# Performance work log

Measured on AMD Instinct MI355X. Metric: run time of the kernel, lower is better.

Reference implementation:

```python
import jax, jax.numpy as jnp
import numpy as np

N = 100000        # nodes
E = 3200000       # random edges (avg degree 32); self-loops added in reference
IN, HID, HEADS, OUT = 10, 32, 2, 4
NEG_SLOPE = 0.2   # PyG GATConv default leaky_relu slope


def setup_inputs() -> dict:
    key = jax.random.key(0)
    ks = jax.random.split(key, 16)
    s = 0.1
    return {
        "x": jax.random.normal(ks[0], (N, IN), jnp.float32),
        "edge_index": jax.random.randint(ks[1], (2, E), 0, N),
        "W1": jax.random.normal(ks[2], (IN, HEADS * HID), jnp.float32) * s,
        "a1s": jax.random.normal(ks[3], (HEADS, HID), jnp.float32) * s,
        "a1d": jax.random.normal(ks[4], (HEADS, HID), jnp.float32) * s,
        "b1": jnp.zeros((HEADS * HID,), jnp.float32),
        "W2": jax.random.normal(ks[5], (HEADS * HID, HEADS * HID), jnp.float32) * s,
        "a2s": jax.random.normal(ks[6], (HEADS, HID), jnp.float32) * s,
        "a2d": jax.random.normal(ks[7], (HEADS, HID), jnp.float32) * s,
        "b2": jnp.zeros((HEADS * HID,), jnp.float32),
        "W3": jax.random.normal(ks[8], (HEADS * HID, OUT), jnp.float32) * s,
        "a3s": jax.random.normal(ks[9], (1, OUT), jnp.float32) * s,
        "a3d": jax.random.normal(ks[10], (1, OUT), jnp.float32) * s,
        "b3": jnp.zeros((OUT,), jnp.float32),
    }


def gat_layer(x, src, dst, W, a_src, a_dst, b, concat):
    """One PyG-style GATConv (shared src/dst linear, self-loops already in src/dst)."""
    heads, oc = a_src.shape
    h = (x @ W).reshape(-1, heads, oc)                    # [N, H, C]
    asc = jnp.einsum('nhc,hc->nh', h, a_src)              # [N, H]
    adc = jnp.einsum('nhc,hc->nh', h, a_dst)              # [N, H]
    e = jax.nn.leaky_relu(asc[src] + adc[dst], NEG_SLOPE) # [Etot, H]
    m = jax.ops.segment_max(e, dst, num_segments=N)       # segment softmax over dst
    ex = jnp.exp(e - m[dst])
    z = jax.ops.segment_sum(ex, dst, num_segments=N)
    alpha = ex / z[dst]                                   # [Etot, H]
    out = jax.ops.segment_sum(h[src] * alpha[:, :, None], dst, num_segments=N)
    out = out.reshape(-1, heads * oc) if concat else out.mean(axis=1)
    return out + b


def reference(x, edge_index, W1, a1s, a1d, b1, W2, a2s, a2d, b2, W3, a3s, a3d, b3):
    loops = jnp.arange(N)
    src = jnp.concatenate([edge_index[0], loops])
    dst = jnp.concatenate([edge_index[1], loops])
    h = jax.nn.relu(gat_layer(x, src, dst, W1, a1s, a1d, b1, True))
    h = jax.nn.relu(gat_layer(h, src, dst, W2, a2s, a2d, b2, True))
    h = gat_layer(h, src, dst, W3, a3s, a3d, b3, False)
    return jax.nn.sigmoid(h) * 100.0
```

## Files before the change

kernel.cpp:

```cpp
#include <hip/hip_runtime.h>
#include <hip/hip_bf16.h>
#include <math.h>

#define NEG_SLOPE 0.2f
#define PSHIFT 8
#define PSIZE 256
#define NPARTS_MAX 392
#define B1 768
#define CELL_CAP 32
#define PCAP 10240
#define LCSR_CAP 10240

typedef int vint2 __attribute__((ext_vector_type(2)));
typedef int vint4 __attribute__((ext_vector_type(4)));
typedef short bf16x8 __attribute__((ext_vector_type(8)));
typedef float floatx4 __attribute__((ext_vector_type(4)));

__device__ __forceinline__ float lrelu(float v) { return fmaxf(v, NEG_SLOPE * v); }

__device__ __forceinline__ unsigned short f2bf(float f) {
    unsigned int b = __float_as_uint(f);
    b += 0x7fffu + ((b >> 16) & 1u);
    return (unsigned short)(b >> 16);
}
__device__ __forceinline__ float bf2f(unsigned short u) {
    return __uint_as_float((unsigned int)u << 16);
}

__global__ void k_part(const int* __restrict__ src, const int* __restrict__ dst, int E,
                       int* __restrict__ pairs, int* __restrict__ ptot, int nparts) {
    __shared__ int stage[NPARTS_MAX * CELL_CAP];
    __shared__ int lcnt[NPARTS_MAX];
    int tid = threadIdx.x, blk = blockIdx.x;
    for (int i = tid; i < nparts; i += 256) lcnt[i] = 0;
    __syncthreads();
    int per = ((E + B1 * 4 - 1) / (B1 * 4)) * 4;
    int s = blk * per, e = min(E, s + per);
    bool al = ((E & 3) == 0);
    for (int i0 = s + tid * 4; i0 < e; i0 += 1024) {
        int dv[4], sv[4], nv;
        if (al && i0 + 4 <= e) {
            vint4 d4 = __builtin_nontemporal_load((const vint4*)(dst + i0));
            vint4 s4 = __builtin_nontemporal_load((const vint4*)(src + i0));
            dv[0] = d4.x; dv[1] = d4.y; dv[2] = d4.z; dv[3] = d4.w;
            sv[0] = s4.x; sv[1] = s4.y; sv[2] = s4.z; sv[3] = s4.w;
            nv = 4;
        } else {
            nv = min(4, e - i0);
            for (int k = 0; k < nv; ++k) {
                dv[k] = __builtin_nontemporal_load(dst + i0 + k);
                sv[k] = __builtin_nontemporal_load(src + i0 + k);
            }
        }
        for (int k = 0; k < nv; ++k) {
            int p = dv[k] >> PSHIFT;
            int pos = atomicAdd(&lcnt[p], 1);
            if (pos < CELL_CAP)
                stage[p * CELL_CAP + pos] = (sv[k] << PSHIFT) | (dv[k] & (PSIZE - 1));
        }
    }
    __syncthreads();
    for (int p = tid; p < nparts; p += 256) {
        int tgt = min(lcnt[p], CELL_CAP);
        if (tgt == 0) continue;
        int base = atomicAdd(&ptot[p], tgt);
        if (base + tgt > PCAP) tgt = max(0, PCAP - base);
        int* gp = pairs + (size_t)p * PCAP + base;
        const int* sp = &stage[p * CELL_CAP];
        for (int j = 0; j < tgt; ++j) gp[j] = sp[j];
    }
}

__global__ void k_pscan(const int* __restrict__ ptot, int* __restrict__ pbase,
                        int* __restrict__ row, int nparts, int N) {
    __shared__ int sh[512];
    int tid = threadIdx.x;
    int v = (tid < nparts) ? min(ptot[tid], PCAP) : 0;
    sh[tid] = v;
    __syncthreads();
    for (int off = 1; off < 512; off <<= 1) {
        int t = (tid >= off) ? sh[tid - off] : 0;
        __syncthreads();
        sh[tid] += t;
        __syncthreads();
    }
    if (tid < nparts) pbase[tid] = sh[tid] - v;
    if (tid == nparts - 1) row[N] = sh[tid];
}

__global__ void k_scat2(const int* __restrict__ pairs, const int* __restrict__ ptot,
                        const int* __restrict__ pbase, int* __restrict__ row,
                        int* __restrict__ csr, int N) {
    __shared__ int lcsr[LCSR_CAP];
    __shared__ int lhist[PSIZE], lcur[PSIZE];
    int part = blockIdx.x;
    int lo = part << PSHIFT;
    int npart = min(PSIZE, N - lo);
    int tid = threadIdx.x;
    int cnt = min(ptot[part], PCAP);
    const int* seg = pairs + (size_t)part * PCAP;
    for (int i = tid; i < PSIZE; i += 1024) lhist[i] = 0;
    __syncthreads();
    for (int i = tid; i < cnt; i += 1024)
        atomicAdd(&lhist[__builtin_nontemporal_load(&seg[i]) & (PSIZE - 1)], 1);
    __syncthreads();
    if (tid < PSIZE) lcur[tid] = lhist[tid];
    __syncthreads();
    for (int off = 1; off < PSIZE; off <<= 1) {
        int t = 0;
        if (tid < PSIZE && tid >= off) t = lcur[tid - off];
        __syncthreads();
        if (tid < PSIZE) lcur[tid] += t;
        __syncthreads();
    }
    int pb = pbase[part];
    if (tid < npart) row[lo + tid] = pb + lcur[tid] - lhist[tid];
    if (tid < PSIZE) lcur[tid] -= lhist[tid];
    __syncthreads();
    for (int i = tid; i < cnt; i += 1024) {
        int v = __builtin_nontemporal_load(&seg[i]);
        int pos = atomicAdd(&lcur[v & (PSIZE - 1)], 1);
        if (pos < LCSR_CAP) lcsr[pos] = (unsigned)v >> PSHIFT;
    }
    __syncthreads();
    for (int i = tid; i < cnt; i += 1024)
        csr[pb + i] = lcsr[i];
}

__global__ void k_lin1(const float* __restrict__ x, const float* __restrict__ W,
                       const float* __restrict__ as_, const float* __restrict__ ad_,
                       unsigned short* __restrict__ hb, float* __restrict__ asc,
                       float* __restrict__ adc, int N) {
    __shared__ float sW[10 * 64];
    int tid = threadIdx.x;
    for (int i = tid; i < 640; i += 256) sW[i] = W[i];
    __syncthreads();
    int wid = tid >> 6, lane = tid & 63;
    int n = blockIdx.x * 4 + wid;
    if (n >= N) return;
    float acc = 0.f;
#pragma unroll
    for (int k = 0; k < 10; ++k) acc += x[n * 10 + k] * sW[k * 64 + lane];
    hb[(size_t)n * 64 + lane] = f2bf(acc);
    int head = lane >> 5, cc = lane & 31;
    float rs = acc * as_[lane];
    float rd = acc * ad_[lane];
#pragma unroll
    for (int m = 16; m >= 1; m >>= 1) {
        rs += __shfl_xor(rs, m, 64);
        rd += __shfl_xor(rd, m, 64);
    }
    if (cc == 0) { asc[n * 2 + head] = rs; adc[n * 2 + head] = rd; }
}

__global__ void k_lin2(const float* __restrict__ yin, const float* __restrict__ W,
                       const float* __restrict__ as_, const float* __restrict__ ad_,
                       unsigned short* __restrict__ hb, float* __restrict__ asc,
                       float* __restrict__ adc, int N) {
    __shared__ unsigned short sW[64 * 64];
    int tid = threadIdx.x;
    for (int i = tid; i < 4096; i += 256) sW[i] = f2bf(W[i]);
    __syncthreads();
    int wid = tid >> 6, lane = tid & 63;
    int quad = lane >> 4, col = lane & 15;
    bf16x8 bfr[4][2];
#pragma unroll
    for (int blk = 0; blk < 4; ++blk)
#pragma unroll
        for (int kh = 0; kh < 2; ++kh)
#pragma unroll
            for (int j = 0; j < 8; ++j)
                bfr[blk][kh][j] = (short)sW[(kh * 32 + quad * 8 + j) * 64 + blk * 16 + col];
    float asv[4], adv[4];
#pragma unroll
    for (int blk = 0; blk < 4; ++blk) {
        asv[blk] = as_[blk * 16 + col];
        adv[blk] = ad_[blk * 16 + col];
    }
    int tile = blockIdx.x * 4 + wid;
    int nb = tile * 16;
    if (nb >= N) return;
    int mrow = nb + col; if (mrow >= N) mrow = N - 1;
    const float* yr = yin + (size_t)mrow * 64;
    bf16x8 afr[2];
#pragma unroll
    for (int kh = 0; kh < 2; ++kh) {
        const floatx4* p = (const floatx4*)(yr + kh * 32 + quad * 8);
        floatx4 u0 = __builtin_nontemporal_load(p);
        floatx4 u1 = __builtin_nontemporal_load(p + 1);
        afr[kh][0] = (short)f2bf(u0[0]); afr[kh][1] = (short)f2bf(u0[1]);
        afr[kh][2] = (short)f2bf(u0[2]); afr[kh][3] = (short)f2bf(u0[3]);
        afr[kh][4] = (short)f2bf(u1[0]); afr[kh][5] = (short)f2bf(u1[1]);
        afr[kh][6] = (short)f2bf(u1[2]); afr[kh][7] = (short)f2bf(u1[3]);
    }
    floatx4 acc[4];
#pragma unroll
    for (int blk = 0; blk < 4; ++blk) {
        acc[blk][0] = 0.f; acc[blk][1] = 0.f; acc[blk][2] = 0.f; acc[blk][3] = 0.f;
        acc[blk] = __builtin_amdgcn_mfma_f32_16x16x32_bf16(afr[0], bfr[blk][0], acc[blk], 0, 0, 0);
        acc[blk] = __builtin_amdgcn_mfma_f32_16x16x32_bf16(afr[1], bfr[blk][1], acc[blk], 0, 0, 0);
    }
#pragma unroll
    for (int r = 0; r < 4; ++r) {
        int m = nb + quad * 4 + r;
        if (m < N) {
#pragma unroll
            for (int blk = 0; blk < 4; ++blk)
                hb[(size_t)m * 64 + blk * 16 + col] = f2bf(acc[blk][r]);
        }
    }
    float s0[4], s1[4], d0[4], d1[4];
#pragma unroll
    for (int r = 0; r < 4; ++r) {
        s0[r] = acc[0][r] * asv[0] + acc[1][r] * asv[1];
        s1[r] = acc[2][r] * asv[2] + acc[3][r] * asv[3];
        d0[r] = acc[0][r] * adv[0] + acc[1][r] * adv[1];
        d1[r] = acc[2][r] * adv[2] + acc[3][r] * adv[3];
    }
#pragma unroll
    for (int mask = 8; mask >= 1; mask >>= 1) {
#pragma unroll
        for (int r = 0; r < 4; ++r) {
            s0[r] += __shfl_xor(s0[r], mask, 64);
            s1[r] += __shfl_xor(s1[r], mask, 64);
            d0[r] += __shfl_xor(d0[r], mask, 64);
            d1[r] += __shfl_xor(d1[r], mask, 64);
        }
    }
    if (col < 4) {
        int m = nb + quad * 4 + col;
        if (m < N) {
            float vs0 = col == 0 ? s0[0] : col == 1 ? s0[1] : col == 2 ? s0[2] : s0[3];
            float vs1 = col == 0 ? s1[0] : col == 1 ? s1[1] : col == 2 ? s1[2] : s1[3];
            float vd0 = col == 0 ? d0[0] : col == 1 ? d0[1] : col == 2 ? d0[2] : d0[3];
            float vd1 = col == 0 ? d1[0] : col == 1 ? d1[1] : col == 2 ? d1[2] : d1[3];
            asc[m * 2 + 0] = vs0; asc[m * 2 + 1] = vs1;
            adc[m * 2 + 0] = vd0; adc[m * 2 + 1] = vd1;
        }
    }
}

__global__ void k_agg(const unsigned short* __restrict__ hb, const float* __restrict__ asc,
                      const float* __restrict__ adc, const int* __restrict__ row,
                      const int* __restrict__ csr_src, const float* __restrict__ bias,
                      float* __restrict__ yout, int N, int do_relu) {
    int tid = threadIdx.x;
    int wid = tid >> 6, lane = tid & 63;
    int n = blockIdx.x * 4 + wid;
    if (n >= N) return;
    int s = row[n], e = row[n + 1];
    int cho = lane & 7;
    int hq = (lane >> 2) & 1;
    int jo = lane >> 3;
    int cho16 = cho << 4;
    float2 ad = ((const float2*)adc)[n];
    float2 asf = ((const float2*)asc)[n];
    float a0 = 0.f, a1 = 0.f, a2 = 0.f, a3 = 0.f;
    float a4 = 0.f, a5 = 0.f, a6 = 0.f, a7 = 0.f;
    float z0 = 0.f, z1 = 0.f;
    const char* hbB = (const char*)hb;
    for (int base = s; base < e; base += 64) {
        int cnt = e - base; if (cnt > 64) cnt = 64;
        int sv7 = 0; float p0 = 0.f, p1 = 0.f;
        if (lane < cnt) {
            int srcv = __builtin_nontemporal_load(csr_src + base + lane);
            float2 av = ((const float2*)asc)[srcv];
            p0 = __expf(lrelu(av.x + ad.x));
            p1 = __expf(lrelu(av.y + ad.y));
            sv7 = srcv << 7;
        }
        z0 += p0; z1 += p1;
#pragma unroll 4
        for (int j = jo; j < cnt; j += 8) {
            int a = __shfl(sv7, j, 64);
            float q0 = __shfl(p0, j, 64);
            float q1 = __shfl(p1, j, 64);
            float p = hq ? q1 : q0;
            vint4 pk = *(const vint4*)(hbB + (unsigned)(a | cho16));
            unsigned int w0 = (unsigned int)pk.x, w1 = (unsigned int)pk.y;
            unsigned int w2 = (unsigned int)pk.z, w3 = (unsigned int)pk.w;
            a0 += p * __uint_as_float(w0 << 16);
            a1 += p * __uint_as_float(w0 & 0xffff0000u);
            a2 += p * __uint_as_float(w1 << 16);
            a3 += p * __uint_as_float(w1 & 0xffff0000u);
            a4 += p * __uint_as_float(w2 << 16);
            a5 += p * __uint_as_float(w2 & 0xffff0000u);
            a6 += p * __uint_as_float(w3 << 16);
            a7 += p * __uint_as_float(w3 & 0xffff0000u);
        }
    }
#pragma unroll
    for (int msk = 8; msk <= 32; msk <<= 1) {
        a0 += __shfl_xor(a0, msk, 64); a1 += __shfl_xor(a1, msk, 64);
        a2 += __shfl_xor(a2, msk, 64); a3 += __shfl_xor(a3, msk, 64);
        a4 += __shfl_xor(a4, msk, 64); a5 += __shfl_xor(a5, msk, 64);
        a6 += __shfl_xor(a6, msk, 64); a7 += __shfl_xor(a7, msk, 64);
    }
#pragma unroll
    for (int msk = 1; msk <= 32; msk <<= 1) {
        z0 += __shfl_xor(z0, msk, 64);
        z1 += __shfl_xor(z1, msk, 64);
    }
    float ps0 = __expf(lrelu(asf.x + ad.x));
    float ps1 = __expf(lrelu(asf.y + ad.y));
    z0 += ps0; z1 += ps1;
    float p_self_my = hq ? ps1 : ps0;
    float zneed = hq ? z1 : z0;
    vint4 pks = *(const vint4*)(hbB + (((unsigned)n << 7) | (unsigned)cho16));
    {
        unsigned int w0 = (unsigned int)pks.x, w1 = (unsigned int)pks.y;
        unsigned int w2 = (unsigned int)pks.z, w3 = (unsigned int)pks.w;
        a0 += p_self_my * __uint_as_float(w0 << 16);
        a1 += p_self_my * __uint_as_float(w0 & 0xffff0000u);
        a2 += p_self_my * __uint_as_float(w1 << 16);
        a3 += p_self_my * __uint_as_float(w1 & 0xffff0000u);
        a4 += p_self_my * __uint_as_float(w2 << 16);
        a5 += p_self_my * __uint_as_float(w2 & 0xffff0000u);
        a6 += p_self_my * __uint_as_float(w3 << 16);
        a7 += p_self_my * __uint_as_float(w3 & 0xffff0000u);
    }
    float inv = 1.f / zneed;
    float4 bv0 = ((const float4*)bias)[cho * 2];
    float4 bv1 = ((const float4*)bias)[cho * 2 + 1];
    float y0 = a0 * inv + bv0.x;
    float y1 = a1 * inv + bv0.y;
    float y2 = a2 * inv + bv0.z;
    float y3 = a3 * inv + bv0.w;
    float y4 = a4 * inv + bv1.x;
    float y5 = a5 * inv + bv1.y;
    float y6 = a6 * inv + bv1.z;
    float y7 = a7 * inv + bv1.w;
    if (do_relu) {
        y0 = fmaxf(y0, 0.f); y1 = fmaxf(y1, 0.f);
        y2 = fmaxf(y2, 0.f); y3 = fmaxf(y3, 0.f);
        y4 = fmaxf(y4, 0.f); y5 = fmaxf(y5, 0.f);
        y6 = fmaxf(y6, 0.f); y7 = fmaxf(y7, 0.f);
    }
    if (jo == 0) {
        floatx4 o0; o0[0] = y0; o0[1] = y1; o0[2] = y2; o0[3] = y3;
        floatx4 o1; o1[0] = y4; o1[1] = y5; o1[2] = y6; o1[3] = y7;
        floatx4* yp = (floatx4*)yout + (size_t)n * 16 + cho * 2;
        __builtin_nontemporal_store(o0, yp);
        __builtin_nontemporal_store(o1, yp + 1);
    }
}

__global__ void k_lin3(const float* __restrict__ yin, const float* __restrict__ W3,
                       const float* __restrict__ a3s, const float* __restrict__ a3d,
                       float4* __restrict__ rec, int N) {
    __shared__ float sW[256];
    int tid = threadIdx.x;
    sW[tid] = W3[tid];
    __syncthreads();
    int t = blockIdx.x * 256 + tid;
    int n = t >> 2, c = t & 3;
    if (n >= N) return;
    float d0 = 0.f, d1 = 0.f, d2 = 0.f, d3 = 0.f;
    const floatx4* yr = (const floatx4*)(yin + (size_t)n * 64 + c * 16);
#pragma unroll
    for (int k4 = 0; k4 < 4; ++k4) {
        floatx4 v = __builtin_nontemporal_load(yr + k4);
        int kb = (c * 16 + k4 * 4) * 4;
        d0 += v[0] * sW[kb + 0];  d1 += v[0] * sW[kb + 1];
        d2 += v[0] * sW[kb + 2];  d3 += v[0] * sW[kb + 3];
        d0 += v[1] * sW[kb + 4];  d1 += v[1] * sW[kb + 5];
        d2 += v[1] * sW[kb + 6];  d3 += v[1] * sW[kb + 7];
        d0 += v[2] * sW[kb + 8];  d1 += v[2] * sW[kb + 9];
        d2 += v[2] * sW[kb + 10]; d3 += v[2] * sW[kb + 11];
        d0 += v[3] * sW[kb + 12]; d1 += v[3] * sW[kb + 13];
        d2 += v[3] * sW[kb + 14]; d3 += v[3] * sW[kb + 15];
    }
    d0 += __shfl_xor(d0, 1, 64); d1 += __shfl_xor(d1, 1, 64);
    d2 += __shfl_xor(d2, 1, 64); d3 += __shfl_xor(d3, 1, 64);
    d0 += __shfl_xor(d0, 2, 64); d1 += __shfl_xor(d1, 2, 64);
    d2 += __shfl_xor(d2, 2, 64); d3 += __shfl_xor(d3, 2, 64);
    if (c == 0) {
        float rs = d0 * a3s[0] + d1 * a3s[1] + d2 * a3s[2] + d3 * a3s[3];
        float rd = d0 * a3d[0] + d1 * a3d[1] + d2 * a3d[2] + d3 * a3d[3];
        unsigned int lo = (unsigned int)f2bf(d0) | ((unsigned int)f2bf(d1) << 16);
        unsigned int hi = (unsigned int)f2bf(d2) | ((unsigned int)f2bf(d3) << 16);
        float4 r;
        r.x = __uint_as_float(lo); r.y = __uint_as_float(hi);
        r.z = rs; r.w = rd;
        rec[n] = r;
    }
}

__global__ void k_agg3(const float4* __restrict__ rec, const int* __restrict__ row,
                       const int* __restrict__ csr_src, const float* __restrict__ b3,
                       float* __restrict__ out, int N) {
    int tid = threadIdx.x;
    int half = tid >> 5, lane = tid & 31;
    int n = blockIdx.x * 8 + half;
    if (n >= N) return;
    int s = row[n], e = row[n + 1];
    float4 rn = rec[n];
    float adcn = rn.w;
    float n0 = 0.f, n1 = 0.f, n2 = 0.f, n3 = 0.f, den = 0.f;
    if (lane == 0) {
        float p = __expf(lrelu(rn.z + adcn));
        unsigned int lo = __float_as_uint(rn.x), hi = __float_as_uint(rn.y);
        n0 = p * __uint_as_float(lo << 16);
        n1 = p * __uint_as_float(lo & 0xffff0000u);
        n2 = p * __uint_as_float(hi << 16);
        n3 = p * __uint_as_float(hi & 0xffff0000u);
        den = p;
    }
    for (int idx = s + lane; idx < e; idx += 32) {
        int src = __builtin_nontemporal_load(csr_src + idx);
        float4 r = rec[src];
        float p = __expf(lrelu(r.z + adcn));
        unsigned int lo = __float_as_uint(r.x), hi = __float_as_uint(r.y);
        n0 += p * __uint_as_float(lo << 16);
        n1 += p * __uint_as_float(lo & 0xffff0000u);
        n2 += p * __uint_as_float(hi << 16);
        n3 += p * __uint_as_float(hi & 0xffff0000u);
        den += p;
    }
#pragma unroll
    for (int msk = 16; msk >= 1; msk >>= 1) {
        n0 += __shfl_xor(n0, msk, 64);
        n1 += __shfl_xor(n1, msk, 64);
        n2 += __shfl_xor(n2, msk, 64);
        n3 += __shfl_xor(n3, msk, 64);
        den += __shfl_xor(den, msk, 64);
    }
    if (lane < 4) {
        float num = lane == 0 ? n0 : lane == 1 ? n1 : lane == 2 ? n2 : n3;
        float v = num / den + b3[lane];
        __builtin_nontemporal_store(100.f / (1.f + __expf(-v)), out + n * 4 + lane);
    }
}

extern "C" void kernel_launch(void* const* d_in, const int* in_sizes, int n_in,
                              void* d_out, int out_size, void* d_ws, size_t ws_size,
                              hipStream_t stream) {
    const float* x   = (const float*)d_in[0];
    const int*   ei  = (const int*)d_in[1];
    const float* W1  = (const float*)d_in[2];
    const float* a1s = (const float*)d_in[3];
    const float* a1d = (const float*)d_in[4];
    const float* b1  = (const float*)d_in[5];
    const float* W2  = (const float*)d_in[6];
    const float* a2s = (const float*)d_in[7];
    const float* a2d = (const float*)d_in[8];
    const float* b2  = (const float*)d_in[9];
    const float* W3  = (const float*)d_in[10];
    const float* a3s = (const float*)d_in[11];
    const float* a3d = (const float*)d_in[12];
    const float* b3  = (const float*)d_in[13];
    float* out = (float*)d_out;

    const int N = in_sizes[0] / 10;
    const int E = in_sizes[1] / 2;
    const int* esrc = ei;
    const int* edst = ei + E;
    const int nparts = (N + PSIZE - 1) >> PSHIFT;

    char* ws = (char*)d_ws;
    size_t off = 0;
    auto alloc = [&](size_t bytes) {
        void* p = ws + off;
        off = (off + bytes + 255) & ~(size_t)255;
        return p;
    };
    int*   row   = (int*)alloc((size_t)(N + 1) * sizeof(int));
    int*   ptot  = (int*)alloc(NPARTS_MAX * sizeof(int));
    int*   pbase = (int*)alloc(NPARTS_MAX * sizeof(int));
    int*   csr   = (int*)alloc((size_t)E * sizeof(int));
    unsigned short* hb = (unsigned short*)alloc((size_t)N * 64 * sizeof(unsigned short));
    float* y     = (float*)alloc((size_t)N * 64 * sizeof(float));
    float4* rec  = (float4*)alloc((size_t)N * sizeof(float4));
    float* asc   = (float*)alloc((size_t)N * 2 * sizeof(float));
    float* adc   = (float*)alloc((size_t)N * 2 * sizeof(float));
    int* pairs = (int*)hb;

    (void)hipMemsetAsync(ptot, 0, NPARTS_MAX * sizeof(int), stream);

    const int nw = (N + 3) / 4;
    const int tiles = (N + 15) / 16;

    k_part<<<B1, 256, 0, stream>>>(esrc, edst, E, pairs, ptot, nparts);
    k_pscan<<<1, 512, 0, stream>>>(ptot, pbase, row, nparts, N);
    k_scat2<<<nparts, 1024, 0, stream>>>(pairs, ptot, pbase, row, csr, N);

    k_lin1<<<nw, 256, 0, stream>>>(x, W1, a1s, a1d, hb, asc, adc, N);
    k_agg<<<nw, 256, 0, stream>>>(hb, asc, adc, row, csr, b1, y, N, 1);
    k_lin2<<<(tiles + 3) / 4, 256, 0, stream>>>(y, W2, a2s, a2d, hb, asc, adc, N);
    k_agg<<<nw, 256, 0, stream>>>(hb, asc, adc, row, csr, b2, y, N, 1);
    k_lin3<<<(N * 4 + 255) / 256, 256, 0, stream>>>(y, W3, a3s, a3d, rec, N);
    k_agg3<<<(N + 7) / 8, 256, 0, stream>>>(rec, row, csr, b3, out, N);
}
```

Measured before the change: 363.2 us.

## Sort CSR neighbors within each row by source-node superblock for gather locality

The per-partition CSR scatter now histograms edges by (destination, source superblock of 4096 nodes) instead of destination only, so each row's neighbor list comes out grouped by source range. The intent is better cache locality for the later gathers of h[src] in the aggregation kernels. In exchange it adds larger shared histograms (two 8192-entry arrays plus a scan buffer), which raise LDS use per block, and a two-level 1024-thread scan in the CSR build.

```diff
diff --git a/kernel.cpp b/kernel.cpp
--- a/kernel.cpp
+++ b/kernel.cpp
@@ -10,6 +10,8 @@
 #define CELL_CAP 32
 #define PCAP 10240
 #define LCSR_CAP 10240
+#define SBSHIFT 12
+#define NSB_MAX 32
 
 typedef int vint2 __attribute__((ext_vector_type(2)));
 typedef int vint4 __attribute__((ext_vector_type(4)));
@@ -90,36 +92,56 @@
 
 __global__ void k_scat2(const int* __restrict__ pairs, const int* __restrict__ ptot,
                         const int* __restrict__ pbase, int* __restrict__ row,
-                        int* __restrict__ csr, int N) {
+                        int* __restrict__ csr, int N, int nsb) {
     __shared__ int lcsr[LCSR_CAP];
-    __shared__ int lhist[PSIZE], lcur[PSIZE];
+    __shared__ int hist2[PSIZE * NSB_MAX];
+    __shared__ int cur2[PSIZE * NSB_MAX];
+    __shared__ int wsum[1024];
     int part = blockIdx.x;
     int lo = part << PSHIFT;
     int npart = min(PSIZE, N - lo);
     int tid = threadIdx.x;
     int cnt = min(ptot[part], PCAP);
     const int* seg = pairs + (size_t)part * PCAP;
-    for (int i = tid; i < PSIZE; i += 1024) lhist[i] = 0;
-    __syncthreads();
-    for (int i = tid; i < cnt; i += 1024)
-        atomicAdd(&lhist[__builtin_nontemporal_load(&seg[i]) & (PSIZE - 1)], 1);
-    __syncthreads();
-    if (tid < PSIZE) lcur[tid] = lhist[tid];
-    __syncthreads();
-    for (int off = 1; off < PSIZE; off <<= 1) {
-        int t = 0;
-        if (tid < PSIZE && tid >= off) t = lcur[tid - off];
-        __syncthreads();
-        if (tid < PSIZE) lcur[tid] += t;
-        __syncthreads();
-    }
-    int pb = pbase[part];
-    if (tid < npart) row[lo + tid] = pb + lcur[tid] - lhist[tid];
-    if (tid < PSIZE) lcur[tid] -= lhist[tid];
+    int nbins = PSIZE * nsb;
+    for (int i = tid; i < nbins; i += 1024) hist2[i] = 0;
     __syncthreads();
     for (int i = tid; i < cnt; i += 1024) {
         int v = __builtin_nontemporal_load(&seg[i]);
-        int pos = atomicAdd(&lcur[v & (PSIZE - 1)], 1);
+        int ldst = v & (PSIZE - 1);
+        int sb = min((int)((unsigned)v >> (PSHIFT + SBSHIFT)), nsb - 1);
+        atomicAdd(&hist2[ldst * nsb + sb], 1);
+    }
+    __syncthreads();
+    int per = (nbins + 1023) >> 10;
+    int b0 = tid * per;
+    int run = 0;
+    for (int k = 0; k < per; ++k) {
+        int b = b0 + k;
+        if (b < nbins) { cur2[b] = run; run += hist2[b]; }
+    }
+    wsum[tid] = run;
+    __syncthreads();
+    for (int off = 1; off < 1024; off <<= 1) {
+        int t = (tid >= off) ? wsum[tid - off] : 0;
+        __syncthreads();
+        wsum[tid] += t;
+        __syncthreads();
+    }
+    int excl = wsum[tid] - run;
+    for (int k = 0; k < per; ++k) {
+        int b = b0 + k;
+        if (b < nbins) cur2[b] += excl;
+    }
+    __syncthreads();
+    int pb = pbase[part];
+    if (tid < npart) row[lo + tid] = pb + cur2[tid * nsb];
+    __syncthreads();
+    for (int i = tid; i < cnt; i += 1024) {
+        int v = __builtin_nontemporal_load(&seg[i]);
+        int ldst = v & (PSIZE - 1);
+        int sb = min((int)((unsigned)v >> (PSHIFT + SBSHIFT)), nsb - 1);
+        int pos = atomicAdd(&cur2[ldst * nsb + sb], 1);
         if (pos < LCSR_CAP) lcsr[pos] = (unsigned)v >> PSHIFT;
     }
     __syncthreads();
@@ -456,6 +478,8 @@
     const int* esrc = ei;
     const int* edst = ei + E;
     const int nparts = (N + PSIZE - 1) >> PSHIFT;
+    int nsb = (N + (1 << SBSHIFT) - 1) >> SBSHIFT;
+    if (nsb > NSB_MAX) nsb = NSB_MAX;
 
     char* ws = (char*)d_ws;
     size_t off = 0;
@@ -482,7 +506,7 @@
 
     k_part<<<B1, 256, 0, stream>>>(esrc, edst, E, pairs, ptot, nparts);
     k_pscan<<<1, 512, 0, stream>>>(ptot, pbase, row, nparts, N);
-    k_scat2<<<nparts, 1024, 0, stream>>>(pairs, ptot, pbase, row, csr, N);
+    k_scat2<<<nparts, 1024, 0, stream>>>(pairs, ptot, pbase, row, csr, N, nsb);
 
     k_lin1<<<nw, 256, 0, stream>>>(x, W1, a1s, a1d, hb, asc, adc, N);
     k_agg<<<nw, 256, 0, stream>>>(hb, asc, adc, row, csr, b1, y, N, 1);
```

Result: slower. 374.6 us (+3.1%).

## Aggregate raw input features before W1 and fuse layer-3 linear into layer-2 aggregation

Applied to the files above, without the earlier changes.

Layer 1 now gathers the 10-dim bf16 input features (padded to 16) instead of the 64-dim projected features, then applies W1 after the softmax-weighted sum, using linearity of the projection. This cuts per-edge gather bytes in the first aggregation by about fourfold. Separately, the layer-2 aggregation computes the layer-3 linear projection and attention scores in-register, removing the k_lin3 kernel and the round trip of the 64-wide intermediate through global memory. The cost is a small per-node matmul epilogue and extra shuffles, plus bf16 rounding of x applied before the projection rather than after.

```diff
diff --git a/kernel.cpp b/kernel.cpp
--- a/kernel.cpp
+++ b/kernel.cpp
@@ -129,7 +129,7 @@
 
 __global__ void k_lin1(const float* __restrict__ x, const float* __restrict__ W,
                        const float* __restrict__ as_, const float* __restrict__ ad_,
-                       unsigned short* __restrict__ hb, float* __restrict__ asc,
+                       unsigned short* __restrict__ xb, float* __restrict__ asc,
                        float* __restrict__ adc, int N) {
     __shared__ float sW[10 * 64];
     int tid = threadIdx.x;
@@ -141,7 +141,10 @@
     float acc = 0.f;
 #pragma unroll
     for (int k = 0; k < 10; ++k) acc += x[n * 10 + k] * sW[k * 64 + lane];
-    hb[(size_t)n * 64 + lane] = f2bf(acc);
+    if (lane < 16) {
+        unsigned short v = (lane < 10) ? f2bf(x[n * 10 + lane]) : (unsigned short)0;
+        xb[(size_t)n * 16 + lane] = v;
+    }
     int head = lane >> 5, cc = lane & 31;
     float rs = acc * as_[lane];
     float rd = acc * ad_[lane];
@@ -151,6 +154,98 @@
         rd += __shfl_xor(rd, m, 64);
     }
     if (cc == 0) { asc[n * 2 + head] = rs; adc[n * 2 + head] = rd; }
+}
+
+__global__ void k_agg1(const unsigned short* __restrict__ xb, const float* __restrict__ x,
+                       const float* __restrict__ asc, const float* __restrict__ adc,
+                       const int* __restrict__ row, const int* __restrict__ csr_src,
+                       const float* __restrict__ W1, const float* __restrict__ b1,
+                       float* __restrict__ yout, int N) {
+    __shared__ float sW[640];
+    int tid = threadIdx.x;
+    for (int i = tid; i < 640; i += 256) sW[i] = W1[i];
+    __syncthreads();
+    int wid = tid >> 6, lane = tid & 63;
+    int n = blockIdx.x * 4 + wid;
+    if (n >= N) return;
+    int s = row[n], e = row[n + 1];
+    int es = lane & 1;
+    int hq = (lane >> 1) & 1;
+    int jo = lane >> 2;
+    int es16 = es << 4;
+    float2 ad = ((const float2*)adc)[n];
+    float2 asf = ((const float2*)asc)[n];
+    float a0 = 0.f, a1 = 0.f, a2 = 0.f, a3 = 0.f;
+    float a4 = 0.f, a5 = 0.f, a6 = 0.f, a7 = 0.f;
+    float z0 = 0.f, z1 = 0.f;
+    const char* xbB = (const char*)xb;
+    for (int base = s; base < e; base += 64) {
+        int cnt = e - base; if (cnt > 64) cnt = 64;
+        int sv5 = 0; float p0 = 0.f, p1 = 0.f;
+        if (lane < cnt) {
+            int srcv = __builtin_nontemporal_load(csr_src + base + lane);
+            float2 av = ((const float2*)asc)[srcv];
+            p0 = __expf(lrelu(av.x + ad.x));
+            p1 = __expf(lrelu(av.y + ad.y));
+            sv5 = srcv << 5;
+        }
+        z0 += p0; z1 += p1;
+#pragma unroll 4
+        for (int j = jo; j < cnt; j += 16) {
+            int a = __shfl(sv5, j, 64);
+            float q0 = __shfl(p0, j, 64);
+            float q1 = __shfl(p1, j, 64);
+            float p = hq ? q1 : q0;
+            vint4 pk = *(const vint4*)(xbB + (unsigned)(a | es16));
+            unsigned int w0 = (unsigned int)pk.x, w1 = (unsigned int)pk.y;
+            unsigned int w2 = (unsigned int)pk.z, w3 = (unsigned int)pk.w;
+            a0 += p * __uint_as_float(w0 << 16);
+            a1 += p * __uint_as_float(w0 & 0xffff0000u);
+            a2 += p * __uint_as_float(w1 << 16);
+            a3 += p * __uint_as_float(w1 & 0xffff0000u);
+            a4 += p * __uint_as_float(w2 << 16);
+            a5 += p * __uint_as_float(w2 & 0xffff0000u);
+            a6 += p * __uint_as_float(w3 << 16);
+            a7 += p * __uint_as_float(w3 & 0xffff0000u);
+        }
+    }
+#pragma unroll
+    for (int msk = 4; msk <= 32; msk <<= 1) {
+        a0 += __shfl_xor(a0, msk, 64); a1 += __shfl_xor(a1, msk, 64);
+        a2 += __shfl_xor(a2, msk, 64); a3 += __shfl_xor(a3, msk, 64);
+        a4 += __shfl_xor(a4, msk, 64); a5 += __shfl_xor(a5, msk, 64);
+        a6 += __shfl_xor(a6, msk, 64); a7 += __shfl_xor(a7, msk, 64);
+    }
+#pragma unroll
+    for (int msk = 1; msk <= 32; msk <<= 1) {
+        z0 += __shfl_xor(z0, msk, 64);
+        z1 += __shfl_xor(z1, msk, 64);
+    }
+    float ps0 = __expf(lrelu(asf.x + ad.x));
+    float ps1 = __expf(lrelu(asf.y + ad.y));
+    z0 += ps0; z1 += ps1;
+    int head = lane >> 5;
+    float psh = head ? ps1 : ps0;
+    float invz = 1.f / (head ? z1 : z0);
+    int l0 = head << 1;
+    float t0 = __shfl(a0, l0, 64), t1 = __shfl(a1, l0, 64);
+    float t2 = __shfl(a2, l0, 64), t3 = __shfl(a3, l0, 64);
+    float t4 = __shfl(a4, l0, 64), t5 = __shfl(a5, l0, 64);
+    float t6 = __shfl(a6, l0, 64), t7 = __shfl(a7, l0, 64);
+    float t8 = __shfl(a0, l0 | 1, 64), t9 = __shfl(a1, l0 | 1, 64);
+    const float* xr = x + (size_t)n * 10;
+    float acc = b1[lane];
+    acc += (t0 + psh * xr[0]) * invz * sW[0 * 64 + lane];
+    acc += (t1 + psh * xr[1]) * invz * sW[1 * 64 + lane];
+    acc += (t2 + psh * xr[2]) * invz * sW[2 * 64 + lane];
+    acc += (t3 + psh * xr[3]) * invz * sW[3 * 64 + lane];
+    acc += (t4 + psh * xr[4]) * invz * sW[4 * 64 + lane];
+    acc += (t5 + psh * xr[5]) * invz * sW[5 * 64 + lane];
+    acc += (t6 + psh * xr[6]) * invz * sW[6 * 64 + lane];
+    acc += (t7 + psh * xr[7]) * invz * sW[7 * 64 + lane];
+    acc += (t8 + psh * xr[8]) * invz * sW[8 * 64 + lane];
+    acc += (t9 + psh * xr[9]) * invz * sW[9 * 64 + lane];
+    yout[(size_t)n * 64 + lane] = fmaxf(acc, 0.f);
 }
 
 __global__ void k_lin2(const float* __restrict__ yin, const float* __restrict__ W,
@@ -240,11 +335,17 @@
     }
 }
 
-__global__ void k_agg(const unsigned short* __restrict__ hb, const float* __restrict__ asc,
-                      const float* __restrict__ adc, const int* __restrict__ row,
-                      const int* __restrict__ csr_src, const float* __restrict__ bias,
-                      float* __restrict__ yout, int N, int do_relu) {
-    int tid = threadIdx.x;
+__global__ void k_agg2(const unsigned short* __restrict__ hb, const float* __restrict__ asc,
+                       const float* __restrict__ adc, const int* __restrict__ row,
+                       const int* __restrict__ csr_src, const float* __restrict__ bias,
+                       const float* __restrict__ W3, const float* __restrict__ a3s,
+                       const float* __restrict__ a3d, float4* __restrict__ rec, int N) {
+    __shared__ float sW3[256];
+    __shared__ float sa3[8];
+    int tid = threadIdx.x;
+    if (tid < 256) sW3[tid] = W3[tid];
+    if (tid < 4) { sa3[tid] = a3s[tid]; sa3[4 + tid] = a3d[tid]; }
+    __syncthreads();
     int wid = tid >> 6, lane = tid & 63;
     int n = blockIdx.x * 4 + wid;
     if (n >= N) return;
@@ -322,61 +423,42 @@
     float inv = 1.f / zneed;
     float4 bv0 = ((const float4*)bias)[cho * 2];
     float4 bv1 = ((const float4*)bias)[cho * 2 + 1];
-    float y0 = a0 * inv + bv0.x;
-    float y1 = a1 * inv + bv0.y;
-    float y2 = a2 * inv + bv0.z;
-    float y3 = a3 * inv + bv0.w;
-    float y4 = a4 * inv + bv1.x;
-    float y5 = a5 * inv + bv1.y;
-    float y6 = a6 * inv + bv1.z;
-    float y7 = a7 * inv + bv1.w;
-    if (do_relu) {
-        y0 = fmaxf(y0, 0.f); y1 = fmaxf(y1, 0.f);
-        y2 = fmaxf(y2, 0.f); y3 = fmaxf(y3, 0.f);
-        y4 = fmaxf(y4, 0.f); y5 = fmaxf(y5, 0.f);
-        y6 = fmaxf(y6, 0.f); y7 = fmaxf(y7, 0.f);
-    }
-    if (jo == 0) {
-        floatx4 o0; o0[0] = y0; o0[1] = y1; o0[2] = y2; o0[3] = y3;
-        floatx4 o1; o1[0] = y4; o1[1] = y5; o1[2] = y6; o1[3] = y7;
-        floatx4* yp = (floatx4*)yout + (size_t)n * 16 + cho * 2;
-        __builtin_nontemporal_store(o0, yp);
-        __builtin_nontemporal_store(o1, yp + 1);
-    }
-}
-
-__global__ void k_lin3(const float* __restrict__ yin, const float* __restrict__ W3,
-                       const float* __restrict__ a3s, const float* __restrict__ a3d,
-                       float4* __restrict__ rec, int N) {
-    __shared__ float sW[256];
-    int tid = threadIdx.x;
-    sW[tid] = W3[tid];
-    __syncthreads();
-    int t = blockIdx.x * 256 + tid;
-    int n = t >> 2, c = t & 3;
-    if (n >= N) return;
+    float y0 = fmaxf(a0 * inv + bv0.x, 0.f);
+    float y1 = fmaxf(a1 * inv + bv0.y, 0.f);
+    float y2 = fmaxf(a2 * inv + bv0.z, 0.f);
+    float y3 = fmaxf(a3 * inv + bv0.w, 0.f);
+    float y4 = fmaxf(a4 * inv + bv1.x, 0.f);
+    float y5 = fmaxf(a5 * inv + bv1.y, 0.f);
+    float y6 = fmaxf(a6 * inv + bv1.z, 0.f);
+    float y7 = fmaxf(a7 * inv + bv1.w, 0.f);
+    int cb = cho * 8;
     float d0 = 0.f, d1 = 0.f, d2 = 0.f, d3 = 0.f;
-    const floatx4* yr = (const floatx4*)(yin + (size_t)n * 64 + c * 16);
-#pragma unroll
-    for (int k4 = 0; k4 < 4; ++k4) {
-        floatx4 v = __builtin_nontemporal_load(yr + k4);
-        int kb = (c * 16 + k4 * 4) * 4;
-        d0 += v[0] * sW[kb + 0];  d1 += v[0] * sW[kb + 1];
-        d2 += v[0] * sW[kb + 2];  d3 += v[0] * sW[kb + 3];
-        d0 += v[1] * sW[kb + 4];  d1 += v[1] * sW[kb + 5];
-        d2 += v[1] * sW[kb + 6];  d3 += v[1] * sW[kb + 7];
-        d0 += v[2] * sW[kb + 8];  d1 += v[2] * sW[kb + 9];
-        d2 += v[2] * sW[kb + 10]; d3 += v[2] * sW[kb + 11];
-        d0 += v[3] * sW[kb + 12]; d1 += v[3] * sW[kb + 13];
-        d2 += v[3] * sW[kb + 14]; d3 += v[3] * sW[kb + 15];
-    }
-    d0 += __shfl_xor(d0, 1, 64); d1 += __shfl_xor(d1, 1, 64);
-    d2 += __shfl_xor(d2, 1, 64); d3 += __shfl_xor(d3, 1, 64);
-    d0 += __shfl_xor(d0, 2, 64); d1 += __shfl_xor(d1, 2, 64);
-    d2 += __shfl_xor(d2, 2, 64); d3 += __shfl_xor(d3, 2, 64);
-    if (c == 0) {
-        float rs = d0 * a3s[0] + d1 * a3s[1] + d2 * a3s[2] + d3 * a3s[3];
-        float rd = d0 * a3d[0] + d1 * a3d[1] + d2 * a3d[2] + d3 * a3d[3];
+    d0 += y0 * sW3[(cb + 0) * 4 + 0]; d1 += y0 * sW3[(cb + 0) * 4 + 1];
+    d2 += y0 * sW3[(cb + 0) * 4 + 2]; d3 += y0 * sW3[(cb + 0) * 4 + 3];
+    d0 += y1 * sW3[(cb + 1) * 4 + 0]; d1 += y1 * sW3[(cb + 1) * 4 + 1];
+    d2 += y1 * sW3[(cb + 1) * 4 + 2]; d3 += y1 * sW3[(cb + 1) * 4 + 3];
+    d0 += y2 * sW3[(cb + 2) * 4 + 0]; d1 += y2 * sW3[(cb + 2) * 4 + 1];
+    d2 += y2 * sW3[(cb + 2) * 4 + 2]; d3 += y2 * sW3[(cb + 2) * 4 + 3];
+    d0 += y3 * sW3[(cb + 3) * 4 + 0]; d1 += y3 * sW3[(cb + 3) * 4 + 1];
+    d2 += y3 * sW3[(cb + 3) * 4 + 2]; d3 += y3 * sW3[(cb + 3) * 4 + 3];
+    d0 += y4 * sW3[(cb + 4) * 4 + 0]; d1 += y4 * sW3[(cb + 4) * 4 + 1];
+    d2 += y4 * sW3[(cb + 4) * 4 + 2]; d3 += y4 * sW3[(cb + 4) * 4 + 3];
+    d0 += y5 * sW3[(cb + 5) * 4 + 0]; d1 += y5 * sW3[(cb + 5) * 4 + 1];
+    d2 += y5 * sW3[(cb + 5) * 4 + 2]; d3 += y5 * sW3[(cb + 5) * 4 + 3];
+    d0 += y6 * sW3[(cb + 6) * 4 + 0]; d1 += y6 * sW3[(cb + 6) * 4 + 1];
+    d2 += y6 * sW3[(cb + 6) * 4 + 2]; d3 += y6 * sW3[(cb + 6) * 4 + 3];
+    d0 += y7 * sW3[(cb + 7) * 4 + 0]; d1 += y7 * sW3[(cb + 7) * 4 + 1];
+    d2 += y7 * sW3[(cb + 7) * 4 + 2]; d3 += y7 * sW3[(cb + 7) * 4 + 3];
+#pragma unroll
+    for (int msk = 1; msk <= 4; msk <<= 1) {
+        d0 += __shfl_xor(d0, msk, 64);
+        d1 += __shfl_xor(d1, msk, 64);
+        d2 += __shfl_xor(d2, msk, 64);
+        d3 += __shfl_xor(d3, msk, 64);
+    }
+    if (lane == 0) {
+        float rs = d0 * sa3[0] + d1 * sa3[1] + d2 * sa3[2] + d3 * sa3[3];
+        float rd = d0 * sa3[4] + d1 * sa3[5] + d2 * sa3[6] + d3 * sa3[7];
         unsigned int lo = (unsigned int)f2bf(d0) | ((unsigned int)f2bf(d1) << 16);
         unsigned int hi = (unsigned int)f2bf(d2) | ((unsigned int)f2bf(d3) << 16);
         float4 r;
@@ -473,6 +555,7 @@
     float4* rec  = (float4*)alloc((size_t)N * sizeof(float4));
     float* asc   = (float*)alloc((size_t)N * 2 * sizeof(float));
     float* adc   = (float*)alloc((size_t)N * 2 * sizeof(float));
+    unsigned short* xb = (unsigned short*)alloc((size_t)N * 16 * sizeof(unsigned short));
     int* pairs = (int*)hb;
 
     (void)hipMemsetAsync(ptot, 0, NPARTS_MAX * sizeof(int), stream);
@@ -484,10 +567,9 @@
     k_pscan<<<1, 512, 0, stream>>>(ptot, pbase, row, nparts, N);
     k_scat2<<<nparts, 1024, 0, stream>>>(pairs, ptot, pbase, row, csr, N);
 
-    k_lin1<<<nw, 256, 0, stream>>>(x, W1, a1s, a1d, hb, asc, adc, N);
-    k_agg<<<nw, 256, 0, stream>>>(hb, asc, adc, row, csr, b1, y, N, 1);
+    k_lin1<<<nw, 256, 0, stream>>>(x, W1, a1s, a1d, xb, asc, adc, N);
+    k_agg1<<<nw, 256, 0, stream>>>(xb, x, asc, adc, row, csr, W1, b1, y, N);
     k_lin2<<<(tiles + 3) / 4, 256, 0, stream>>>(y, W2, a2s, a2d, hb, asc, adc, N);
-    k_agg<<<nw, 256, 0, stream>>>(hb, asc, adc, row, csr, b2, y, N, 1);
-    k_lin3<<<(N * 4 + 255) / 256, 256, 0, stream>>>(y, W3, a3s, a3d, rec, N);
+    k_agg2<<<nw, 256, 0, stream>>>(hb, asc, adc, row, csr, b2, W3, a3s, a3d, rec, N);
     k_agg3<<<(N + 7) / 8, 256, 0, stream>>>(rec, row, csr, b3, out, N);
 }
```

Result: slower. 387.4 us (+6.7%).
